# Optimization experiments

Hardware: AMD Instinct MI355X
Metric: run time of the kernel (lower is better)

The kernel has to match this reference:

```python
import jax, jax.numpy as jnp
import numpy as np

N_HEADS = 16


def setup_inputs() -> dict:
    key = jax.random.key(0)
    ks = jax.random.split(key, 9)
    B, S, D = 2, 2048, 2048
    s = 0.02
    return {
        "X": jax.random.normal(ks[0], (B, S, D), jnp.float32),
        "Wq": jax.random.normal(ks[1], (D, D), jnp.float32) * s,
        "bq": jax.random.normal(ks[2], (D,), jnp.float32) * s,
        "Wk": jax.random.normal(ks[3], (D, D), jnp.float32) * s,
        "bk": jax.random.normal(ks[4], (D,), jnp.float32) * s,
        "Wv": jax.random.normal(ks[5], (D, D), jnp.float32) * s,
        "bv": jax.random.normal(ks[6], (D,), jnp.float32) * s,
        "Wo": jax.random.normal(ks[7], (D, D), jnp.float32) * s,
        "bo": jax.random.normal(ks[8], (D,), jnp.float32) * s,
    }


def reference(X, Wq, bq, Wk, bk, Wv, bv, Wo, bo):
    B, S, D = X.shape
    H = N_HEADS
    d_head = D // H
    # qk_scale = 1/sqrt(sqrt(d_head)), applied to BOTH Q and K
    scale = jnp.asarray(1.0 / np.sqrt(np.sqrt(d_head)), X.dtype)
    Q = (X @ Wq.T + bq).reshape(B, S, H, d_head) * scale  # bqhd
    K = (X @ Wk.T + bk).reshape(B, S, H, d_head) * scale  # bkhd
    V = (X @ Wv.T + bv).reshape(B, S, H, d_head)          # bkhd
    scores = jnp.einsum("bqhd,bkhd->bhqk", Q, K)
    causal = jnp.tril(jnp.ones((S, S), bool))  # [q, k]
    scores = jnp.where(causal[None, None], scores, -jnp.inf)
    # original casts logits to fp32 before softmax, back to Q dtype after
    attn = jax.nn.softmax(scores.astype(jnp.float32), axis=-1).astype(X.dtype)
    out = jnp.einsum("bhqk,bkhd->bqhd", attn, V).reshape(B, S, D)
    return out @ Wo.T + bo
```

## Files before the change

### kernel.cpp

```cpp
#include <hip/hip_runtime.h>


typedef __attribute__((ext_vector_type(8))) short bfx8;
typedef __attribute__((ext_vector_type(4))) float f32x4;

#define TO_GLOBAL(p) ((const __attribute__((address_space(1))) void*)(p))
#define TO_LDS(p)    ((__attribute__((address_space(3))) void*)(p))

__device__ __forceinline__ unsigned short f2bf(float f) {
    unsigned int u = __float_as_uint(f);
    u += 0x7FFFu + ((u >> 16) & 1u);
    return (unsigned short)(u >> 16);
}

__device__ __forceinline__ void store_out(unsigned short* p, float v) { *p = f2bf(v); }
__device__ __forceinline__ void store_out(float* p, float v) { *p = v; }

__global__ void cast_bf16_kernel(const float* __restrict__ x,
                                 unsigned short* __restrict__ y, int n4) {
    int i = blockIdx.x * blockDim.x + threadIdx.x;
    int st = gridDim.x * blockDim.x;
    for (; i < n4; i += st) {
        float4 v = reinterpret_cast<const float4*>(x)[i];
        ushort4 o;
        o.x = f2bf(v.x); o.y = f2bf(v.y); o.z = f2bf(v.z); o.w = f2bf(v.w);
        reinterpret_cast<ushort4*>(y)[i] = o;
    }
}

__global__ void cast3_kernel(const float* __restrict__ s0, const float* __restrict__ s1,
                             const float* __restrict__ s2,
                             unsigned short* __restrict__ d0, unsigned short* __restrict__ d1,
                             unsigned short* __restrict__ d2, int n4) {
    const float* s = (blockIdx.y == 0) ? s0 : (blockIdx.y == 1) ? s1 : s2;
    unsigned short* d = (blockIdx.y == 0) ? d0 : (blockIdx.y == 1) ? d1 : d2;
    int i = blockIdx.x * blockDim.x + threadIdx.x;
    int st = gridDim.x * blockDim.x;
    for (; i < n4; i += st) {
        float4 v = reinterpret_cast<const float4*>(s)[i];
        ushort4 o;
        o.x = f2bf(v.x); o.y = f2bf(v.y); o.z = f2bf(v.z); o.w = f2bf(v.w);
        reinterpret_cast<ushort4*>(d)[i] = o;
    }
}

__device__ __forceinline__ void xcd_swizzle_16x32(int& bx, int& by) {
    const int lin = by * 16 + bx;
    const int wl  = (lin & 7) * 64 + (lin >> 3);
    bx = wl & 15;
    by = wl >> 4;
}

template <typename OUT>
__global__ __launch_bounds__(256) void gemm_bt(
    const unsigned short* __restrict__ A, const unsigned short* __restrict__ Bw,
    const float* __restrict__ bias, OUT* __restrict__ C,
    int M, int N, int K, float scale) {
    __shared__ __align__(16) unsigned short Ash[128 * 32];
    __shared__ __align__(16) unsigned short Bsh[128 * 32];

    const int tid  = threadIdx.x;
    const int lane = tid & 63;
    const int w    = tid >> 6;
    const int g    = lane >> 4;
    const int l15  = lane & 15;
    int bx = blockIdx.x, by = blockIdx.y;
    xcd_swizzle_16x32(bx, by);
    const int m0   = by * 128;
    const int n0   = bx * 128;
    const int wm   = (w >> 1) * 64;
    const int wn   = (w & 1) * 64;

    f32x4 acc[4][4];
#pragma unroll
    for (int i = 0; i < 4; i++)
#pragma unroll
        for (int j = 0; j < 4; j++) acc[i][j] = (f32x4){0.f, 0.f, 0.f, 0.f};

    const int c0 = tid, c1 = tid + 256;
    const int rowA0 = c0 >> 2, colA0 = (c0 & 3) * 8;
    const int rowA1 = c1 >> 2, colA1 = (c1 & 3) * 8;

    for (int k0 = 0; k0 < K; k0 += 32) {
        __syncthreads();
        __builtin_amdgcn_global_load_lds(TO_GLOBAL(A + (size_t)(m0 + rowA0) * K + k0 + colA0),
                                         TO_LDS(&Ash[c0 * 8]), 16, 0, 0);
        __builtin_amdgcn_global_load_lds(TO_GLOBAL(A + (size_t)(m0 + rowA1) * K + k0 + colA1),
                                         TO_LDS(&Ash[c1 * 8]), 16, 0, 0);
        __builtin_amdgcn_global_load_lds(TO_GLOBAL(Bw + (size_t)(n0 + rowA0) * K + k0 + colA0),
                                         TO_LDS(&Bsh[c0 * 8]), 16, 0, 0);
        __builtin_amdgcn_global_load_lds(TO_GLOBAL(Bw + (size_t)(n0 + rowA1) * K + k0 + colA1),
                                         TO_LDS(&Bsh[c1 * 8]), 16, 0, 0);
        __syncthreads();

        bfx8 af[4], bfr[4];
#pragma unroll
        for (int mi = 0; mi < 4; mi++)
            af[mi] = *reinterpret_cast<const bfx8*>(&Ash[(wm + mi * 16 + l15) * 32 + g * 8]);
#pragma unroll
        for (int ni = 0; ni < 4; ni++)
            bfr[ni] = *reinterpret_cast<const bfx8*>(&Bsh[(wn + ni * 16 + l15) * 32 + g * 8]);
#pragma unroll
        for (int mi = 0; mi < 4; mi++)
#pragma unroll
            for (int ni = 0; ni < 4; ni++)
                acc[mi][ni] = __builtin_amdgcn_mfma_f32_16x16x32_bf16(af[mi], bfr[ni],
                                                                     acc[mi][ni], 0, 0, 0);
    }

#pragma unroll
    for (int mi = 0; mi < 4; mi++) {
#pragma unroll
        for (int ni = 0; ni < 4; ni++) {
            const int col = n0 + wn + ni * 16 + l15;
            const float bv = bias[col];
#pragma unroll
            for (int r = 0; r < 4; r++) {
                const int row = m0 + wm + mi * 16 + g * 4 + r;
                store_out(&C[(size_t)row * N + col], (acc[mi][ni][r] + bv) * scale);
            }
        }
    }
}

__global__ __launch_bounds__(256) void gemm_qkv(
    const unsigned short* __restrict__ A,
    const unsigned short* __restrict__ W0, const unsigned short* __restrict__ W1,
    const unsigned short* __restrict__ W2,
    const float* __restrict__ b0, const float* __restrict__ b1,
    const float* __restrict__ b2,
    unsigned short* __restrict__ C0, unsigned short* __restrict__ C1,
    unsigned short* __restrict__ C2, float qks) {
    const int z = blockIdx.z;
    const unsigned short* Bw = (z == 0) ? W0 : (z == 1) ? W1 : W2;
    const float* bias = (z == 0) ? b0 : (z == 1) ? b1 : b2;
    unsigned short* C = (z == 0) ? C0 : (z == 1) ? C1 : C2;
    const float scale = (z < 2) ? qks : 1.0f;
    const int N = 2048, K = 2048;

    __shared__ __align__(16) unsigned short Ash[128 * 32];
    __shared__ __align__(16) unsigned short Bsh[128 * 32];

    const int tid  = threadIdx.x;
    const int lane = tid & 63;
    const int w    = tid >> 6;
    const int g    = lane >> 4;
    const int l15  = lane & 15;
    int bx = blockIdx.x, by = blockIdx.y;
    xcd_swizzle_16x32(bx, by);
    const int m0   = by * 128;
    const int n0   = bx * 128;
    const int wm   = (w >> 1) * 64;
    const int wn   = (w & 1) * 64;

    f32x4 acc[4][4];
#pragma unroll
    for (int i = 0; i < 4; i++)
#pragma unroll
        for (int j = 0; j < 4; j++) acc[i][j] = (f32x4){0.f, 0.f, 0.f, 0.f};

    const int c0 = tid, c1 = tid + 256;
    const int rowA0 = c0 >> 2, colA0 = (c0 & 3) * 8;
    const int rowA1 = c1 >> 2, colA1 = (c1 & 3) * 8;

    for (int k0 = 0; k0 < K; k0 += 32) {
        __syncthreads();
        __builtin_amdgcn_global_load_lds(TO_GLOBAL(A + (size_t)(m0 + rowA0) * K + k0 + colA0),
                                         TO_LDS(&Ash[c0 * 8]), 16, 0, 0);
        __builtin_amdgcn_global_load_lds(TO_GLOBAL(A + (size_t)(m0 + rowA1) * K + k0 + colA1),
                                         TO_LDS(&Ash[c1 * 8]), 16, 0, 0);
        __builtin_amdgcn_global_load_lds(TO_GLOBAL(Bw + (size_t)(n0 + rowA0) * K + k0 + colA0),
                                         TO_LDS(&Bsh[c0 * 8]), 16, 0, 0);
        __builtin_amdgcn_global_load_lds(TO_GLOBAL(Bw + (size_t)(n0 + rowA1) * K + k0 + colA1),
                                         TO_LDS(&Bsh[c1 * 8]), 16, 0, 0);
        __syncthreads();

        bfx8 af[4], bfr[4];
#pragma unroll
        for (int mi = 0; mi < 4; mi++)
            af[mi] = *reinterpret_cast<const bfx8*>(&Ash[(wm + mi * 16 + l15) * 32 + g * 8]);
#pragma unroll
        for (int ni = 0; ni < 4; ni++)
            bfr[ni] = *reinterpret_cast<const bfx8*>(&Bsh[(wn + ni * 16 + l15) * 32 + g * 8]);
#pragma unroll
        for (int mi = 0; mi < 4; mi++)
#pragma unroll
            for (int ni = 0; ni < 4; ni++)
                acc[mi][ni] = __builtin_amdgcn_mfma_f32_16x16x32_bf16(af[mi], bfr[ni],
                                                                     acc[mi][ni], 0, 0, 0);
    }

    if (z == 2) {
#pragma unroll
        for (int mi = 0; mi < 4; mi++) {
            const int rbase = m0 + wm + mi * 16 + g * 4;
            const int b_ = rbase >> 11;
            const int sbase = rbase & 2047;
#pragma unroll
            for (int ni = 0; ni < 4; ni++) {
                const int col = n0 + wn + ni * 16 + l15;
                const float bv = bias[col];
                ushort4 o;
                o.x = f2bf(acc[mi][ni][0] + bv);
                o.y = f2bf(acc[mi][ni][1] + bv);
                o.z = f2bf(acc[mi][ni][2] + bv);
                o.w = f2bf(acc[mi][ni][3] + bv);
                *reinterpret_cast<ushort4*>(C + ((size_t)(b_ * 2048 + col)) * 2048 + sbase) = o;
            }
        }
    } else {
#pragma unroll
        for (int mi = 0; mi < 4; mi++) {
#pragma unroll
            for (int ni = 0; ni < 4; ni++) {
                const int col = n0 + wn + ni * 16 + l15;
                const float bv = bias[col];
#pragma unroll
                for (int r = 0; r < 4; r++) {
                    const int row = m0 + wm + mi * 16 + g * 4 + r;
                    C[(size_t)row * N + col] = f2bf((acc[mi][ni][r] + bv) * scale);
                }
            }
        }
    }
}

#define SLEN 2048
#define DMODEL 2048
#define M2FIX 11.541560327f

__global__ __launch_bounds__(256, 3) void attn_kernel(
    const unsigned short* __restrict__ Q, const unsigned short* __restrict__ Kp,
    const unsigned short* __restrict__ Vt, unsigned short* __restrict__ O) {
    __shared__ __align__(16) unsigned short Ksh[64 * 128];
    __shared__ __align__(16) unsigned short Vsh[128 * 64];
    __shared__ __align__(16) unsigned short Psh[4 * 1024];

    const int tid  = threadIdx.x;
    const int lane = tid & 63;
    const int w    = tid >> 6;
    const int g    = lane >> 4;
    const int l15  = lane & 15;
    const int bh   = blockIdx.x;
    const int b    = bh >> 4, h = bh & 15;
    const int pr   = blockIdx.y;

    const size_t bhbase = (size_t)b * SLEN * DMODEL + (size_t)h * 128;
    const size_t vtbase = (size_t)bh * 128 * SLEN;

    unsigned short* Pw = &Psh[w * 1024];
    const int khi_b = l15 >> 3, klo = l15 & 7;
    const int vsw = l15 & 7;

    const int krow = tid >> 4, kch = tid & 15;
    const int vdr  = tid >> 3, vch = tid & 7;

    bfx8 kreg[4], vreg[4];

#define LOADREGS(KB)                                                                \
    {                                                                               \
        _Pragma("unroll")                                                           \
        for (int i_ = 0; i_ < 4; i_++)                                              \
            kreg[i_] = *reinterpret_cast<const bfx8*>(                              \
                Kp + bhbase + (size_t)((KB) + krow + 16 * i_) * DMODEL + kch * 8);  \
        _Pragma("unroll")                                                           \
        for (int i_ = 0; i_ < 4; i_++)                                              \
            vreg[i_] = *reinterpret_cast<const bfx8*>(                              \
                Vt + vtbase + (size_t)(vdr + 32 * i_) * SLEN + (KB) + vch * 8);     \
    }

#pragma unroll 1
    for (int seg = 0; seg < 2; seg++) {
        const int qt  = seg == 0 ? (31 - pr) : pr;
        const int q0w = qt * 64 + w * 16;

        bfx8 qf[4];
#pragma unroll
        for (int c = 0; c < 4; c++)
            qf[c] = *reinterpret_cast<const bfx8*>(
                Q + bhbase + (size_t)(q0w + l15) * DMODEL + c * 32 + g * 8);

        f32x4 oacc[8];
#pragma unroll
        for (int i = 0; i < 8; i++) oacc[i] = (f32x4){0.f, 0.f, 0.f, 0.f};
        float lpart[4] = {0.f, 0.f, 0.f, 0.f};

        const int ntile = qt + 1;
        LOADREGS(0);

#pragma unroll 1
        for (int t = 0; t < ntile; t++) {
            const int kb = t * 64;
            __builtin_amdgcn_s_barrier();
            __builtin_amdgcn_sched_barrier(0);
#pragma unroll
            for (int i = 0; i < 4; i++) {
                const int row = krow + 16 * i;
                *reinterpret_cast<bfx8*>(&Ksh[row * 128 + ((kch ^ (row & 7)) * 8)]) = kreg[i];
            }
#pragma unroll
            for (int i = 0; i < 4; i++) {
                const int dr = vdr + 32 * i;
                *reinterpret_cast<bfx8*>(&Vsh[dr * 64 + ((vch ^ (dr & 7)) * 8)]) = vreg[i];
            }
            asm volatile("s_waitcnt lgkmcnt(0)" ::: "memory");
            __builtin_amdgcn_s_barrier();
            __builtin_amdgcn_sched_barrier(0);
            if (t + 1 < ntile) LOADREGS(kb + 64);

            __builtin_amdgcn_s_setprio(1);
            f32x4 sacc[4];
#pragma unroll
            for (int kt = 0; kt < 4; kt++) sacc[kt] = (f32x4){0.f, 0.f, 0.f, 0.f};
#pragma unroll
            for (int kt = 0; kt < 4; kt++) {
                const int row = kt * 16 + l15;
#pragma unroll
                for (int c = 0; c < 4; c++) {
                    bfx8 kf = *reinterpret_cast<const bfx8*>(
                        &Ksh[row * 128 + (((c * 4 + g) ^ (row & 7)) * 8)]);
                    sacc[kt] = __builtin_amdgcn_mfma_f32_16x16x32_bf16(
                        qf[c], kf, sacc[kt], 0, 0, 0);
                }
            }
            __builtin_amdgcn_s_setprio(0);
            if (t == ntile - 1) {
#pragma unroll
                for (int kt = 0; kt < 4; kt++)
#pragma unroll
                    for (int r = 0; r < 4; r++)
                        if (kb + kt * 16 + l15 > q0w + g * 4 + r)
                            sacc[kt][r] = -1e30f;
            }
#pragma unroll
            for (int r = 0; r < 4; r++) {
                const float p0 = exp2f(sacc[0][r] - M2FIX);
                const float p1 = exp2f(sacc[1][r] - M2FIX);
                const float p2 = exp2f(sacc[2][r] - M2FIX);
                const float p3 = exp2f(sacc[3][r] - M2FIX);
                lpart[r] += (p0 + p1) + (p2 + p3);
                const int ql = g * 4 + r;
                const int swz = ql & 7;
                Pw[ql * 64 + (((khi_b + 0) ^ swz) << 3) + klo] = f2bf(p0);
                Pw[ql * 64 + (((khi_b + 2) ^ swz) << 3) + klo] = f2bf(p1);
                Pw[ql * 64 + (((khi_b + 4) ^ swz) << 3) + klo] = f2bf(p2);
                Pw[ql * 64 + (((khi_b + 6) ^ swz) << 3) + klo] = f2bf(p3);
            }
            __builtin_amdgcn_s_setprio(1);
#pragma unroll
            for (int ks = 0; ks < 2; ks++) {
                bfx8 vb[8];
#pragma unroll
                for (int ni = 0; ni < 8; ni++) {
                    const int d = ni * 16 + l15;
                    vb[ni] = *reinterpret_cast<const bfx8*>(
                        &Vsh[d * 64 + (((ks * 4 + g) ^ vsw) * 8)]);
                }
                bfx8 pa = *reinterpret_cast<const bfx8*>(
                    Pw + l15 * 64 + (((ks * 4 + g) ^ vsw) << 3));
#pragma unroll
                for (int ni = 0; ni < 8; ni++)
                    oacc[ni] = __builtin_amdgcn_mfma_f32_16x16x32_bf16(
                        pa, vb[ni], oacc[ni], 0, 0, 0);
            }
            __builtin_amdgcn_s_setprio(0);
        }

#pragma unroll
        for (int r = 0; r < 4; r++) {
            float l = lpart[r];
#pragma unroll
            for (int s = 1; s < 16; s <<= 1) l += __shfl_xor(l, s);
            const float inv = 1.0f / l;
            const int q = q0w + g * 4 + r;
#pragma unroll
            for (int ni = 0; ni < 8; ni++)
                O[bhbase + (size_t)q * DMODEL + ni * 16 + l15] = f2bf(oacc[ni][r] * inv);
        }
    }
#undef LOADREGS
}

extern "C" void kernel_launch(void* const* d_in, const int* in_sizes, int n_in,
                              void* d_out, int out_size, void* d_ws, size_t ws_size,
                              hipStream_t stream) {
    const float* X  = (const float*)d_in[0];
    const float* Wq = (const float*)d_in[1];
    const float* bq = (const float*)d_in[2];
    const float* Wk = (const float*)d_in[3];
    const float* bk = (const float*)d_in[4];
    const float* Wv = (const float*)d_in[5];
    const float* bv = (const float*)d_in[6];
    const float* Wo = (const float*)d_in[7];
    const float* bo = (const float*)d_in[8];
    float* out = (float*)d_out;

    unsigned short* ws  = (unsigned short*)d_ws;
    unsigned short* Qb  = ws;
    unsigned short* Kb  = ws + 8388608;
    unsigned short* Vtb = ws + 16777216;
    unsigned short* XOb = ws + 25165824;
    unsigned short* Wb  = ws + 33554432;
    unsigned short* out_u = (unsigned short*)d_out;
    unsigned short* Wkb   = out_u;
    unsigned short* Wvb   = out_u + 4194304;

    const float qk_scale = 0.35709585f;

    const dim3 cb(256);

    cast_bf16_kernel<<<dim3(2048), cb, 0, stream>>>(X, XOb, 2097152);
    cast3_kernel<<<dim3(1024, 3), cb, 0, stream>>>(Wq, Wk, Wv, Wb, Wkb, Wvb, 1048576);

    gemm_qkv<<<dim3(16, 32, 3), cb, 0, stream>>>(XOb, Wb, Wkb, Wvb, bq, bk, bv,
                                                 Qb, Kb, Vtb, qk_scale);

    attn_kernel<<<dim3(32, 16), cb, 0, stream>>>(Qb, Kb, Vtb, XOb);

    cast_bf16_kernel<<<dim3(1024), cb, 0, stream>>>(Wo, Wb, 1048576);
    gemm_bt<float><<<dim3(16, 32), cb, 0, stream>>>(XOb, Wb, bo, out, 4096, 2048, 2048, 1.0f);
}
```

Baseline: 288.3 us.

## Stage transposed V epilogue through swizzled LDS and drop XCD block swizzle

The V projection epilogue now writes its tile into a reused, XOR-swizzled LDS buffer and reads it back transposed, so each thread issues 16-byte contiguous stores along the sequence dimension instead of scattered 8-byte stores. Separately, the XCD-aware block index remapping is removed from both GEMM kernels, so blocks map directly to tiles. The transpose adds extra barriers and LDS traffic in the epilogue. Removing the swizzle may hurt L2 locality across XCDs.

```diff
diff --git a/kernel.cpp b/kernel.cpp
--- a/kernel.cpp
+++ b/kernel.cpp
@@ -44,13 +44,6 @@
     }
 }
 
-__device__ __forceinline__ void xcd_swizzle_16x32(int& bx, int& by) {
-    const int lin = by * 16 + bx;
-    const int wl  = (lin & 7) * 64 + (lin >> 3);
-    bx = wl & 15;
-    by = wl >> 4;
-}
-
 template <typename OUT>
 __global__ __launch_bounds__(256) void gemm_bt(
     const unsigned short* __restrict__ A, const unsigned short* __restrict__ Bw,
@@ -64,10 +57,8 @@
     const int w    = tid >> 6;
     const int g    = lane >> 4;
     const int l15  = lane & 15;
-    int bx = blockIdx.x, by = blockIdx.y;
-    xcd_swizzle_16x32(bx, by);
-    const int m0   = by * 128;
-    const int n0   = bx * 128;
+    const int m0   = blockIdx.y * 128;
+    const int n0   = blockIdx.x * 128;
     const int wm   = (w >> 1) * 64;
     const int wn   = (w & 1) * 64;
 
@@ -138,18 +129,17 @@
     const float scale = (z < 2) ? qks : 1.0f;
     const int N = 2048, K = 2048;
 
-    __shared__ __align__(16) unsigned short Ash[128 * 32];
-    __shared__ __align__(16) unsigned short Bsh[128 * 32];
+    __shared__ __align__(16) unsigned short S[8192];
+    unsigned short* Ash = S;
+    unsigned short* Bsh = S + 4096;
 
     const int tid  = threadIdx.x;
     const int lane = tid & 63;
     const int w    = tid >> 6;
     const int g    = lane >> 4;
     const int l15  = lane & 15;
-    int bx = blockIdx.x, by = blockIdx.y;
-    xcd_swizzle_16x32(bx, by);
-    const int m0   = by * 128;
-    const int n0   = bx * 128;
+    const int m0   = blockIdx.y * 128;
+    const int n0   = blockIdx.x * 128;
     const int wm   = (w >> 1) * 64;
     const int wn   = (w & 1) * 64;
 
@@ -191,22 +181,42 @@
     }
 
     if (z == 2) {
-#pragma unroll
-        for (int mi = 0; mi < 4; mi++) {
-            const int rbase = m0 + wm + mi * 16 + g * 4;
-            const int b_ = rbase >> 11;
-            const int sbase = rbase & 2047;
-#pragma unroll
-            for (int ni = 0; ni < 4; ni++) {
-                const int col = n0 + wn + ni * 16 + l15;
-                const float bv = bias[col];
-                ushort4 o;
-                o.x = f2bf(acc[mi][ni][0] + bv);
-                o.y = f2bf(acc[mi][ni][1] + bv);
-                o.z = f2bf(acc[mi][ni][2] + bv);
-                o.w = f2bf(acc[mi][ni][3] + bv);
-                *reinterpret_cast<ushort4*>(C + ((size_t)(b_ * 2048 + col)) * 2048 + sbase) = o;
-            }
+        __syncthreads();
+        unsigned short (*T)[128] = reinterpret_cast<unsigned short(*)[128]>(S);
+        const int b_ = m0 >> 11;
+        const int sb0 = m0 & 2047;
+        const int td  = tid >> 1;
+        const int ts0 = (tid & 1) * 32;
+        unsigned short* dst0 = C + ((size_t)(b_ * 2048 + n0 + td)) * 2048 + sb0 + ts0;
+#pragma unroll
+        for (int h = 0; h < 2; ++h) {
+            if ((w >> 1) == h) {
+#pragma unroll
+                for (int mi = 0; mi < 4; mi++) {
+#pragma unroll
+                    for (int ni = 0; ni < 4; ni++) {
+                        const int col = wn + ni * 16 + l15;
+                        const float bv = bias[n0 + col];
+#pragma unroll
+                        for (int r = 0; r < 4; r++) {
+                            const int s = mi * 16 + g * 4 + r;
+                            T[s][col ^ ((s & 7) << 3)] = f2bf(acc[mi][ni][r] + bv);
+                        }
+                    }
+                }
+            }
+            __syncthreads();
+#pragma unroll
+            for (int i = 0; i < 4; ++i) {
+                bfx8 o;
+#pragma unroll
+                for (int j = 0; j < 8; ++j) {
+                    const int s = ts0 + i * 8 + j;
+                    o[j] = (short)T[s][td ^ ((s & 7) << 3)];
+                }
+                *reinterpret_cast<bfx8*>(dst0 + h * 64 + i * 8) = o;
+            }
+            __syncthreads();
         }
     } else {
 #pragma unroll
```

Result: no change. 292.7 us (+1.5%).
